# Optimization experiments

Measured on AMD Instinct MI355X. Metric: run time of the kernel, lower is better.

The kernel has to match this reference:

```python
import math
import jax, jax.numpy as jnp
import numpy as np

B, L, D = 8, 512, 1024
H, HD = 16, 64  # num_heads, head_dim (proj_dim = D)
ALPHA = 0.02       # target_alpha, warmup_steps=0 -> alpha_eff = 0.02 (< max_alpha)
STEPS = 4          # diffusion_steps
EPS = 1e-6         # _eps for float32
EARLY = 1e-5       # early_stop_eps
TEMP = 1.0

def setup_inputs() -> dict:
    key = jax.random.key(0)
    ks = jax.random.split(key, 5)
    def w(k):
        return jax.random.normal(k, (D, D), jnp.float32) * 0.02
    return {
        "hidden_states": jax.random.normal(ks[0], (B, L, D), jnp.float32),
        "Wq": w(ks[1]), "bq": jnp.zeros((D,), jnp.float32),
        "Wk": w(ks[2]), "bk": jnp.zeros((D,), jnp.float32),
        "Wv": w(ks[3]), "bv": jnp.zeros((D,), jnp.float32),
        "Wo": w(ks[4]), "bo": jnp.zeros((D,), jnp.float32),
    }

def _forward(hidden_states, Wq, bq, Wk, bk, Wv, bv, Wo, bo):
    Bn, Lq, _ = hidden_states.shape
    # projections -> (B, H, L, HD)
    Q = (hidden_states @ Wq + bq).reshape(Bn, Lq, H, HD).transpose(0, 2, 1, 3)
    K = (hidden_states @ Wk + bk).reshape(Bn, Lq, H, HD).transpose(0, 2, 1, 3)
    V = (hidden_states @ Wv + bv).reshape(Bn, Lq, H, HD).transpose(0, 2, 1, 3)
    # baseline attention p0 (no mask)
    scores = jnp.einsum('bhqd,bhkd->bhqk', Q, K) / math.sqrt(HD)
    p0 = jax.nn.softmax(scores, axis=-1)
    # key-based transition matrix P (cosine similarity, full mode)
    Kn = K / jnp.maximum(jnp.linalg.norm(K, axis=-1, keepdims=True), EPS)
    sim = jnp.einsum('bhid,bhjd->bhij', Kn, Kn) / max(1.0, math.sqrt(HD)) / TEMP
    P = jax.nn.softmax(sim, axis=-1)
    P = P * (1.0 - EPS) + EPS / P.shape[-1]  # jitter
    # iterative diffusion: p <- (1-a)*p0 + a * p @ P, with early stopping
    p = p0
    prev = p0
    done = jnp.array(False)
    for i in range(STEPS):
        p_next = (1.0 - ALPHA) * p0 + ALPHA * jnp.einsum('bhqk,bhkj->bhqj', p, P)
        if i == 0:
            cond = jnp.array(False)
        else:
            cond = jnp.max(jnp.abs(p_next - prev)) < EARLY
        new_p = jnp.where(done, p, p_next)
        new_prev = jnp.where(done | cond, prev, p)
        done = done | cond
        p, prev = new_p, new_prev
    # attention output
    attn = jnp.einsum('bhqk,bhkd->bhqd', p, V)
    attn = attn.transpose(0, 2, 1, 3).reshape(Bn, Lq, H * HD)
    return attn @ Wo + bo

def reference(hidden_states, Wq, bq, Wk, bk, Wv, bv, Wo, bo):
    return _forward(hidden_states, Wq, bq, Wk, bk, Wv, bv, Wo, bo)
```

## Files before the change

### kernel.cpp

```cpp
#include <hip/hip_runtime.h>
#include <stdint.h>

#define B_ 8
#define L_ 512
#define D_ 1024
#define H_ 16
#define HD_ 64
#define BH_ (B_*H_)
#define NR_ (B_*L_)
#define ALPHA_ 0.02f
#define PSTR 72

typedef unsigned int u32;
typedef unsigned short u16;
typedef __attribute__((ext_vector_type(8))) short bf16x8;
typedef __attribute__((ext_vector_type(4))) float f32x4;

#define MFMA16(a, b, c) __builtin_amdgcn_mfma_f32_16x16x32_bf16((a), (b), (c), 0, 0, 0)

__device__ __forceinline__ u32 f2bf_rne(float f) {
    u32 x = __float_as_uint(f);
    return (x + 0x7fffu + ((x >> 16) & 1u)) >> 16;
}
__device__ __forceinline__ float bf_lo(u32 u) { return __uint_as_float(u << 16); }
__device__ __forceinline__ float bf_hi(u32 u) { return __uint_as_float(u & 0xffff0000u); }

__device__ __forceinline__ void pack4_store(float4 v, u16* p) {
    uint2 u;
    u.x = f2bf_rne(v.x) | (f2bf_rne(v.y) << 16);
    u.y = f2bf_rne(v.z) | (f2bf_rne(v.w) << 16);
    *(uint2*)p = u;
}

__device__ __forceinline__ void gl_lds16(const u16* g, u16* l) {
    auto gp = reinterpret_cast<const __attribute__((address_space(1))) void*>(
        reinterpret_cast<uintptr_t>(g));
    auto lp = reinterpret_cast<__attribute__((address_space(3))) void*>(
        reinterpret_cast<uintptr_t>(l));
    __builtin_amdgcn_global_load_lds(gp, lp, 16, 0, 0);
}

__device__ __forceinline__ void stage8_swz(const u16* g, size_t gpitch, u16* lds, int lane) {
    const int lrow = lane >> 3;
    const int su = (lane & 7) ^ lrow;
    gl_lds16(&g[(size_t)lrow * gpitch + su * 8], lds);
}

__global__ __launch_bounds__(256) void cast_bf16(
    const float* __restrict__ src, u16* __restrict__ dst, int n8)
{
    int i = blockIdx.x * 256 + threadIdx.x;
    if (i < n8) {
        float4 a = ((const float4*)src)[(size_t)i * 2];
        float4 b = ((const float4*)src)[(size_t)i * 2 + 1];
        uint4 o;
        o.x = f2bf_rne(a.x) | (f2bf_rne(a.y) << 16);
        o.y = f2bf_rne(a.z) | (f2bf_rne(a.w) << 16);
        o.z = f2bf_rne(b.x) | (f2bf_rne(b.y) << 16);
        o.w = f2bf_rne(b.z) | (f2bf_rne(b.w) << 16);
        ((uint4*)dst)[i] = o;
    }
}

__global__ __launch_bounds__(256) void wT_bf16(
    const float* __restrict__ W0, const float* __restrict__ W1,
    const float* __restrict__ W2, const float* __restrict__ W3,
    u16* __restrict__ WTh)
{
    __shared__ float Ws[64][65];
    const int wsel = blockIdx.z;
    const float* W = (wsel == 0) ? W0 : (wsel == 1) ? W1 : (wsel == 2) ? W2 : W3;
    const int k0 = blockIdx.x * 64, n0 = blockIdx.y * 64;
    const int t = threadIdx.x;
    {
        const int r = t >> 2, c0 = (t & 3) << 4;
        #pragma unroll
        for (int i = 0; i < 4; ++i)
            *(float4*)&Ws[r][c0 + i * 4] = *(const float4*)&W[(size_t)(k0 + r) * 1024 + n0 + c0 + i * 4];
    }
    __syncthreads();
    {
        const int n = t >> 2, kc0 = (t & 3) << 4;
        size_t base = ((size_t)wsel << 20) + (size_t)(n0 + n) * 1024 + k0 + kc0;
        #pragma unroll
        for (int j = 0; j < 4; ++j) {
            float4 v;
            v.x = Ws[kc0 + j * 4 + 0][n]; v.y = Ws[kc0 + j * 4 + 1][n];
            v.z = Ws[kc0 + j * 4 + 2][n]; v.w = Ws[kc0 + j * 4 + 3][n];
            pack4_store(v, &WTh[base + j * 4]);
        }
    }
}

template<int TERMS>
__global__ __launch_bounds__(256) void gemm_mfma(
    const u16* __restrict__ Ah, const u16* __restrict__ Al,
    const u16* __restrict__ WTh,
    const float* __restrict__ b0, const float* __restrict__ b1, const float* __restrict__ b2,
    float* __restrict__ Cf, u16* __restrict__ Ch,
    u16* __restrict__ Kn, u16* __restrict__ VdT, int qkv_mode)
{
    __shared__ u16 Ash[128 * 64];
    __shared__ u16 Als[TERMS == 2 ? 128 * 64 : 8];
    __shared__ u16 Bsh[128 * 64];
    const int bm = blockIdx.x;
    const int which = blockIdx.y >> 3;
    const int bn = blockIdx.y & 7;
    const float* bias = (which == 0) ? b0 : (which == 1) ? b1 : b2;
    const int t = threadIdx.x;
    const int w = t >> 6, lane = t & 63, l15 = lane & 15, g = lane >> 4;
    const int wr = w >> 1, wc = w & 1;
    const int row0 = bm * 128, col0 = bn * 128;
    const u16* Bg = WTh + ((size_t)which << 20);
    const int r7 = l15 & 7;

    f32x4 acc[4][4];
    #pragma unroll
    for (int i = 0; i < 4; ++i)
        #pragma unroll
        for (int j = 0; j < 4; ++j) acc[i][j] = (f32x4){0.f, 0.f, 0.f, 0.f};

    for (int kt = 0; kt < 1024; kt += 64) {
        __syncthreads();
        #pragma unroll
        for (int q = 0; q < 4; ++q) {
            const int rb = w * 32 + q * 8;
            stage8_swz(&Ah[(size_t)(row0 + rb) * 1024 + kt], 1024, &Ash[rb * 64], lane);
            if constexpr (TERMS == 2)
                stage8_swz(&Al[(size_t)(row0 + rb) * 1024 + kt], 1024, &Als[rb * 64], lane);
            stage8_swz(&Bg[(size_t)(col0 + rb) * 1024 + kt], 1024, &Bsh[rb * 64], lane);
        }
        __syncthreads();
        #pragma unroll
        for (int c = 0; c < 2; ++c) {
            const int uo = ((c * 4 + g) ^ r7) * 8;
            bf16x8 ah[4], al[4], bh[4];
            #pragma unroll
            for (int mf = 0; mf < 4; ++mf) {
                const int ro = (wr * 64 + mf * 16 + l15) * 64 + uo;
                ah[mf] = *(const bf16x8*)&Ash[ro];
                if constexpr (TERMS == 2) al[mf] = *(const bf16x8*)&Als[ro];
            }
            #pragma unroll
            for (int nf = 0; nf < 4; ++nf)
                bh[nf] = *(const bf16x8*)&Bsh[(wc * 64 + nf * 16 + l15) * 64 + uo];
            #pragma unroll
            for (int mf = 0; mf < 4; ++mf)
                #pragma unroll
                for (int nf = 0; nf < 4; ++nf) {
                    acc[mf][nf] = MFMA16(ah[mf], bh[nf], acc[mf][nf]);
                    if constexpr (TERMS == 2)
                        acc[mf][nf] = MFMA16(al[mf], bh[nf], acc[mf][nf]);
                }
        }
    }

    if (!qkv_mode) {
        #pragma unroll
        for (int mf = 0; mf < 4; ++mf)
            #pragma unroll
            for (int nf = 0; nf < 4; ++nf) {
                const int n = col0 + wc * 64 + nf * 16 + l15;
                const float bv = bias[n];
                #pragma unroll
                for (int r = 0; r < 4; ++r) {
                    const int m = row0 + wr * 64 + mf * 16 + g * 4 + r;
                    Cf[(size_t)m * 1024 + n] = acc[mf][nf][r] + bv;
                }
            }
        return;
    }
    if (which == 0) {
        #pragma unroll
        for (int mf = 0; mf < 4; ++mf)
            #pragma unroll
            for (int nf = 0; nf < 4; ++nf) {
                const int n = col0 + wc * 64 + nf * 16 + l15;
                const float bv = bias[n];
                #pragma unroll
                for (int r = 0; r < 4; ++r) {
                    const int m = row0 + wr * 64 + mf * 16 + g * 4 + r;
                    Ch[(size_t)m * 1024 + n] = (u16)f2bf_rne(acc[mf][nf][r] + bv);
                }
            }
    } else if (which == 1) {
        #pragma unroll
        for (int mf = 0; mf < 4; ++mf) {
            float v[4][4];
            float sq[4] = {0.f, 0.f, 0.f, 0.f};
            #pragma unroll
            for (int nf = 0; nf < 4; ++nf) {
                const int n = col0 + wc * 64 + nf * 16 + l15;
                const float bv = bias[n];
                #pragma unroll
                for (int r = 0; r < 4; ++r) {
                    v[nf][r] = acc[mf][nf][r] + bv;
                    sq[r] += v[nf][r] * v[nf][r];
                }
            }
            #pragma unroll
            for (int r = 0; r < 4; ++r) {
                sq[r] += __shfl_xor(sq[r], 1);
                sq[r] += __shfl_xor(sq[r], 2);
                sq[r] += __shfl_xor(sq[r], 4);
                sq[r] += __shfl_xor(sq[r], 8);
            }
            float rn[4];
            #pragma unroll
            for (int r = 0; r < 4; ++r)
                rn[r] = 1.f / fmaxf(sqrtf(sq[r]), 1e-6f);
            #pragma unroll
            for (int nf = 0; nf < 4; ++nf) {
                const int n = col0 + wc * 64 + nf * 16 + l15;
                #pragma unroll
                for (int r = 0; r < 4; ++r) {
                    const int m = row0 + wr * 64 + mf * 16 + g * 4 + r;
                    Ch[((size_t)1 << 22) + (size_t)m * 1024 + n] = (u16)f2bf_rne(v[nf][r]);
                    Kn[(size_t)m * 1024 + n] = (u16)f2bf_rne(v[nf][r] * rn[r]);
                }
            }
        }
    } else {
        #pragma unroll
        for (int mf = 0; mf < 4; ++mf) {
            const int m0 = row0 + wr * 64 + mf * 16 + g * 4;
            const int bb = m0 >> 9, l0v = m0 & 511;
            #pragma unroll
            for (int nf = 0; nf < 4; ++nf) {
                const int n = col0 + wc * 64 + nf * 16 + l15;
                const float bv = bias[n];
                const int hh = n >> 6, dd = n & 63;
                const size_t idx = (((size_t)(bb * 16 + hh) * 64 + dd) * 512) + l0v;
                uint2 u;
                u.x = f2bf_rne(acc[mf][nf][0] + bv) | (f2bf_rne(acc[mf][nf][1] + bv) << 16);
                u.y = f2bf_rne(acc[mf][nf][2] + bv) | (f2bf_rne(acc[mf][nf][3] + bv) << 16);
                *(uint2*)&VdT[idx] = u;
            }
        }
    }
}

__global__ __launch_bounds__(256) void qgfd_mfma(
    const u16* __restrict__ Kn_g, const u16* __restrict__ VdT,
    u16* __restrict__ WhT)
{
    __shared__ u16 Rs[64 * 64];
    __shared__ u16 Js[64 * 64];
    __shared__ u16 Vs[64 * 64];
    __shared__ u16 Eh[4][16 * PSTR];
    const int bh = blockIdx.y, b = bh >> 4, h = bh & 15;
    const int r0 = blockIdx.x * 64;
    const int t = threadIdx.x;
    const int w = t >> 6, lane = t & 63, l15 = lane & 15, g = lane >> 4;
    const int r7 = l15 & 7;

    #pragma unroll
    for (int q = 0; q < 2; ++q) {
        const int rb = w * 16 + q * 8;
        stage8_swz(&Kn_g[((size_t)(b * 512 + r0 + rb)) * 1024 + h * 64], 1024,
                   &Rs[rb * 64], lane);
    }
    __syncthreads();
    bf16x8 rbf[2];
    rbf[0] = *(const bf16x8*)&Rs[(w * 16 + l15) * 64 + ((g ^ r7) * 8)];
    rbf[1] = *(const bf16x8*)&Rs[(w * 16 + l15) * 64 + (((4 + g) ^ r7) * 8)];

    float rsum = 0.f;
    f32x4 O[4] = {{0,0,0,0},{0,0,0,0},{0,0,0,0},{0,0,0,0}};

    for (int jt = 0; jt < 512; jt += 64) {
        __syncthreads();
        #pragma unroll
        for (int q = 0; q < 2; ++q) {
            const int rb = w * 16 + q * 8;
            stage8_swz(&Kn_g[((size_t)(b * 512 + jt + rb)) * 1024 + h * 64], 1024,
                       &Js[rb * 64], lane);
            stage8_swz(&VdT[((size_t)(bh * 64 + rb)) * 512 + jt], 512,
                       &Vs[rb * 64], lane);
        }
        __syncthreads();
        #pragma unroll
        for (int tk = 0; tk < 4; ++tk) {
            f32x4 a = {0.f, 0.f, 0.f, 0.f};
            #pragma unroll
            for (int c = 0; c < 2; ++c) {
                bf16x8 ka = *(const bf16x8*)&Js[(tk * 16 + l15) * 64 + (((c * 4 + g) ^ r7) * 8)];
                a = MFMA16(ka, rbf[c], a);
            }
            const float e0 = __expf(a[0] * 0.125f);
            const float e1 = __expf(a[1] * 0.125f);
            const float e2 = __expf(a[2] * 0.125f);
            const float e3 = __expf(a[3] * 0.125f);
            rsum += e0 + e1 + e2 + e3;
            uint2 u;
            u.x = f2bf_rne(e0) | (f2bf_rne(e1) << 16);
            u.y = f2bf_rne(e2) | (f2bf_rne(e3) << 16);
            *(uint2*)&Eh[w][l15 * PSTR + tk * 16 + g * 4] = u;
        }
        bf16x8 pah[2];
        pah[0] = *(const bf16x8*)&Eh[w][l15 * PSTR + 8 * g];
        pah[1] = *(const bf16x8*)&Eh[w][l15 * PSTR + 32 + 8 * g];
        #pragma unroll
        for (int td = 0; td < 4; ++td) {
            #pragma unroll
            for (int c = 0; c < 2; ++c) {
                bf16x8 vb = *(const bf16x8*)&Vs[(td * 16 + l15) * 64 + (((c * 4 + g) ^ r7) * 8)];
                O[td] = MFMA16(pah[c], vb, O[td]);
            }
        }
    }
    rsum += __shfl_xor(rsum, 16);
    rsum += __shfl_xor(rsum, 32);
    const float dinv = (1.0f - 1e-6f) / rsum;
    float dv[4];
    #pragma unroll
    for (int r = 0; r < 4; ++r) dv[r] = __shfl(dinv, g * 4 + r) * ALPHA_;
    #pragma unroll
    for (int td = 0; td < 4; ++td) {
        const int d = td * 16 + l15;
        const size_t idx = ((size_t)bh * 64 + d) * 512 + r0 + w * 16 + g * 4;
        uint2 vv = *(const uint2*)&VdT[idx];
        uint2 wu;
        wu.x = f2bf_rne((1.0f - ALPHA_) * bf_lo(vv.x) + dv[0] * O[td][0])
             | (f2bf_rne((1.0f - ALPHA_) * bf_hi(vv.x) + dv[1] * O[td][1]) << 16);
        wu.y = f2bf_rne((1.0f - ALPHA_) * bf_lo(vv.y) + dv[2] * O[td][2])
             | (f2bf_rne((1.0f - ALPHA_) * bf_hi(vv.y) + dv[3] * O[td][3]) << 16);
        *(uint2*)&WhT[idx] = wu;
    }
}

__global__ __launch_bounds__(256) void attn_mfma(
    const u16* __restrict__ Qh_g, const u16* __restrict__ Kh_g,
    const u16* __restrict__ Wh_g,
    u16* __restrict__ attnh, u16* __restrict__ attnl)
{
    __shared__ u16 Qs[64 * 64];
    __shared__ u16 Ks[64 * 64];
    __shared__ u16 Wsh[64 * 64];
    __shared__ u16 Ph[4][16 * PSTR];
    const int bh = blockIdx.y, b = bh >> 4, h = bh & 15;
    const int q0 = blockIdx.x * 64;
    const int t = threadIdx.x;
    const int w = t >> 6, lane = t & 63, l15 = lane & 15, g = lane >> 4;
    const int r7 = l15 & 7;

    #pragma unroll
    for (int q = 0; q < 2; ++q) {
        const int rb = w * 16 + q * 8;
        stage8_swz(&Qh_g[((size_t)(b * 512 + q0 + rb)) * 1024 + h * 64], 1024,
                   &Qs[rb * 64], lane);
    }
    __syncthreads();
    bf16x8 qbh[2];
    qbh[0] = *(const bf16x8*)&Qs[(w * 16 + l15) * 64 + ((g ^ r7) * 8)];
    qbh[1] = *(const bf16x8*)&Qs[(w * 16 + l15) * 64 + (((4 + g) ^ r7) * 8)];

    float m_run = -1e30f, l_run = 0.f;
    f32x4 O[4] = {{0,0,0,0},{0,0,0,0},{0,0,0,0},{0,0,0,0}};

    for (int kt = 0; kt < 512; kt += 64) {
        __syncthreads();
        #pragma unroll
        for (int q = 0; q < 2; ++q) {
            const int rb = w * 16 + q * 8;
            stage8_swz(&Kh_g[((size_t)(b * 512 + kt + rb)) * 1024 + h * 64], 1024,
                       &Ks[rb * 64], lane);
            stage8_swz(&Wh_g[((size_t)(bh * 64 + rb)) * 512 + kt], 512,
                       &Wsh[rb * 64], lane);
        }
        __syncthreads();
        f32x4 st[4];
        #pragma unroll
        for (int tk = 0; tk < 4; ++tk) {
            f32x4 a = {0.f, 0.f, 0.f, 0.f};
            #pragma unroll
            for (int c = 0; c < 2; ++c) {
                bf16x8 kah = *(const bf16x8*)&Ks[(tk * 16 + l15) * 64 + (((c * 4 + g) ^ r7) * 8)];
                a = MFMA16(kah, qbh[c], a);
            }
            st[tk] = a;
        }
        float mt = st[0][0];
        #pragma unroll
        for (int tk = 0; tk < 4; ++tk)
            #pragma unroll
            for (int r = 0; r < 4; ++r) mt = fmaxf(mt, st[tk][r]);
        mt = fmaxf(mt, __shfl_xor(mt, 16));
        mt = fmaxf(mt, __shfl_xor(mt, 32));
        const float m_new = fmaxf(m_run, mt);
        const float scale = __expf((m_run - m_new) * 0.125f);
        float rsum = 0.f;
        #pragma unroll
        for (int tk = 0; tk < 4; ++tk) {
            float p0_ = __expf((st[tk][0] - m_new) * 0.125f);
            float p1_ = __expf((st[tk][1] - m_new) * 0.125f);
            float p2_ = __expf((st[tk][2] - m_new) * 0.125f);
            float p3_ = __expf((st[tk][3] - m_new) * 0.125f);
            rsum += p0_ + p1_ + p2_ + p3_;
            uint2 hw;
            hw.x = f2bf_rne(p0_) | (f2bf_rne(p1_) << 16);
            hw.y = f2bf_rne(p2_) | (f2bf_rne(p3_) << 16);
            *(uint2*)&Ph[w][l15 * PSTR + tk * 16 + g * 4] = hw;
        }
        rsum += __shfl_xor(rsum, 16);
        rsum += __shfl_xor(rsum, 32);
        l_run = l_run * scale + rsum;
        m_run = m_new;
        float sc[4];
        #pragma unroll
        for (int r = 0; r < 4; ++r) sc[r] = __shfl(scale, g * 4 + r);
        #pragma unroll
        for (int td = 0; td < 4; ++td)
            #pragma unroll
            for (int r = 0; r < 4; ++r) O[td][r] *= sc[r];
        bf16x8 pah[2];
        pah[0] = *(const bf16x8*)&Ph[w][l15 * PSTR + 8 * g];
        pah[1] = *(const bf16x8*)&Ph[w][l15 * PSTR + 32 + 8 * g];
        #pragma unroll
        for (int td = 0; td < 4; ++td) {
            #pragma unroll
            for (int c = 0; c < 2; ++c) {
                bf16x8 wbh = *(const bf16x8*)&Wsh[(td * 16 + l15) * 64 + (((c * 4 + g) ^ r7) * 8)];
                O[td] = MFMA16(pah[c], wbh, O[td]);
            }
        }
    }
    const float linv = 1.f / l_run;
    float li[4];
    #pragma unroll
    for (int r = 0; r < 4; ++r) li[r] = __shfl(linv, g * 4 + r);
    #pragma unroll
    for (int td = 0; td < 4; ++td)
        #pragma unroll
        for (int r = 0; r < 4; ++r) {
            const float v = O[td][r] * li[r];
            const size_t idx = ((size_t)(b * 512 + q0 + w * 16 + g * 4 + r)) * 1024
                             + h * 64 + td * 16 + l15;
            const u32 hh = f2bf_rne(v);
            attnh[idx] = (u16)hh;
            attnl[idx] = (u16)f2bf_rne(v - bf_lo(hh));
        }
}

extern "C" void kernel_launch(void* const* d_in, const int* in_sizes, int n_in,
                              void* d_out, int out_size, void* d_ws, size_t ws_size,
                              hipStream_t stream) {
    const float* X  = (const float*)d_in[0];
    const float* Wq = (const float*)d_in[1];
    const float* bq = (const float*)d_in[2];
    const float* Wk = (const float*)d_in[3];
    const float* bk = (const float*)d_in[4];
    const float* Wv = (const float*)d_in[5];
    const float* bv = (const float*)d_in[6];
    const float* Wo = (const float*)d_in[7];
    const float* bo = (const float*)d_in[8];
    float* out = (float*)d_out;

    char* ws = (char*)d_ws;
    size_t off = 0;
    auto alloc = [&](size_t bytes) -> void* {
        void* p = ws + off;
        off += (bytes + 255) & ~(size_t)255;
        return p;
    };
    const size_t NE = (size_t)NR_ * D_;
    const size_t HE = (size_t)BH_ * 64 * 512;
    u16*   Xh    = (u16*)alloc(NE * 2);
    u16*   WTh   = (u16*)alloc((size_t)4 * 1024 * 1024 * 2);
    u16*   QKh   = (u16*)alloc(2 * NE * 2);
    u16*   Kn    = (u16*)alloc(NE * 2);
    u16*   VdT   = (u16*)alloc(HE * 2);
    u16*   WhT   = (u16*)alloc(HE * 2);
    u16*   attnh = (u16*)alloc(NE * 2);
    u16*   attnl = (u16*)alloc(NE * 2);

    const u16* Qh_g = QKh;
    const u16* Kh_g = QKh + NE;

    dim3 blk(256);
    cast_bf16<<<dim3(2048), blk, 0, stream>>>(X, Xh, (int)(NE / 8));
    wT_bf16<<<dim3(16, 16, 4), blk, 0, stream>>>(Wq, Wk, Wv, Wo, WTh);
    gemm_mfma<1><<<dim3(32, 24), blk, 0, stream>>>(Xh, nullptr, WTh, bq, bk, bv,
                                                   nullptr, QKh, Kn, VdT, 1);
    qgfd_mfma<<<dim3(8, BH_), blk, 0, stream>>>(Kn, VdT, WhT);
    attn_mfma<<<dim3(8, BH_), blk, 0, stream>>>(Qh_g, Kh_g, WhT, attnh, attnl);
    gemm_mfma<2><<<dim3(32, 8), blk, 0, stream>>>(attnh, attnl,
                                                  WTh + ((size_t)3 << 20),
                                                  bo, bo, bo, out, nullptr,
                                                  nullptr, nullptr, 0);
}
```

Measured before the change: 140.1 us.

## Process 128 rows per block in diffusion and attention kernels; fuse prep casts

```diff
diff --git a/kernel.cpp b/kernel.cpp
--- a/kernel.cpp
+++ b/kernel.cpp
@@ -46,32 +46,33 @@
     gl_lds16(&g[(size_t)lrow * gpitch + su * 8], lds);
 }
 
-__global__ __launch_bounds__(256) void cast_bf16(
-    const float* __restrict__ src, u16* __restrict__ dst, int n8)
-{
-    int i = blockIdx.x * 256 + threadIdx.x;
-    if (i < n8) {
-        float4 a = ((const float4*)src)[(size_t)i * 2];
-        float4 b = ((const float4*)src)[(size_t)i * 2 + 1];
-        uint4 o;
-        o.x = f2bf_rne(a.x) | (f2bf_rne(a.y) << 16);
-        o.y = f2bf_rne(a.z) | (f2bf_rne(a.w) << 16);
-        o.z = f2bf_rne(b.x) | (f2bf_rne(b.y) << 16);
-        o.w = f2bf_rne(b.z) | (f2bf_rne(b.w) << 16);
-        ((uint4*)dst)[i] = o;
-    }
-}
-
-__global__ __launch_bounds__(256) void wT_bf16(
+__global__ __launch_bounds__(256) void prep_kernel(
+    const float* __restrict__ X, u16* __restrict__ Xh,
     const float* __restrict__ W0, const float* __restrict__ W1,
     const float* __restrict__ W2, const float* __restrict__ W3,
     u16* __restrict__ WTh)
 {
+    const int t = threadIdx.x;
+    if (blockIdx.z == 4) {
+        const int cid = blockIdx.y * 16 + blockIdx.x;
+        #pragma unroll
+        for (int i = 0; i < 8; ++i) {
+            const int n8 = cid * 2048 + i * 256 + t;
+            float4 a = ((const float4*)X)[(size_t)n8 * 2];
+            float4 b = ((const float4*)X)[(size_t)n8 * 2 + 1];
+            uint4 o;
+            o.x = f2bf_rne(a.x) | (f2bf_rne(a.y) << 16);
+            o.y = f2bf_rne(a.z) | (f2bf_rne(a.w) << 16);
+            o.z = f2bf_rne(b.x) | (f2bf_rne(b.y) << 16);
+            o.w = f2bf_rne(b.z) | (f2bf_rne(b.w) << 16);
+            ((uint4*)Xh)[n8] = o;
+        }
+        return;
+    }
     __shared__ float Ws[64][65];
     const int wsel = blockIdx.z;
     const float* W = (wsel == 0) ? W0 : (wsel == 1) ? W1 : (wsel == 2) ? W2 : W3;
     const int k0 = blockIdx.x * 64, n0 = blockIdx.y * 64;
-    const int t = threadIdx.x;
     {
         const int r = t >> 2, c0 = (t & 3) << 4;
         #pragma unroll
@@ -244,29 +245,33 @@
     const u16* __restrict__ Kn_g, const u16* __restrict__ VdT,
     u16* __restrict__ WhT)
 {
-    __shared__ u16 Rs[64 * 64];
+    __shared__ u16 Rs[128 * 64];
     __shared__ u16 Js[64 * 64];
     __shared__ u16 Vs[64 * 64];
     __shared__ u16 Eh[4][16 * PSTR];
     const int bh = blockIdx.y, b = bh >> 4, h = bh & 15;
-    const int r0 = blockIdx.x * 64;
+    const int r0 = blockIdx.x * 128;
     const int t = threadIdx.x;
     const int w = t >> 6, lane = t & 63, l15 = lane & 15, g = lane >> 4;
     const int r7 = l15 & 7;
 
     #pragma unroll
-    for (int q = 0; q < 2; ++q) {
-        const int rb = w * 16 + q * 8;
+    for (int q = 0; q < 4; ++q) {
+        const int rb = w * 32 + q * 8;
         stage8_swz(&Kn_g[((size_t)(b * 512 + r0 + rb)) * 1024 + h * 64], 1024,
                    &Rs[rb * 64], lane);
     }
     __syncthreads();
-    bf16x8 rbf[2];
-    rbf[0] = *(const bf16x8*)&Rs[(w * 16 + l15) * 64 + ((g ^ r7) * 8)];
-    rbf[1] = *(const bf16x8*)&Rs[(w * 16 + l15) * 64 + (((4 + g) ^ r7) * 8)];
-
-    float rsum = 0.f;
-    f32x4 O[4] = {{0,0,0,0},{0,0,0,0},{0,0,0,0},{0,0,0,0}};
+    bf16x8 rbf[2][2];
+    #pragma unroll
+    for (int rt = 0; rt < 2; ++rt) {
+        rbf[rt][0] = *(const bf16x8*)&Rs[(rt * 64 + w * 16 + l15) * 64 + ((g ^ r7) * 8)];
+        rbf[rt][1] = *(const bf16x8*)&Rs[(rt * 64 + w * 16 + l15) * 64 + (((4 + g) ^ r7) * 8)];
+    }
+
+    float rsum[2] = {0.f, 0.f};
+    f32x4 O[2][4] = {{{0,0,0,0},{0,0,0,0},{0,0,0,0},{0,0,0,0}},
+                     {{0,0,0,0},{0,0,0,0},{0,0,0,0},{0,0,0,0}}};
 
     for (int jt = 0; jt < 512; jt += 64) {
         __syncthreads();
@@ -280,52 +285,59 @@
         }
         __syncthreads();
         #pragma unroll
-        for (int tk = 0; tk < 4; ++tk) {
-            f32x4 a = {0.f, 0.f, 0.f, 0.f};
-            #pragma unroll
-            for (int c = 0; c < 2; ++c) {
-                bf16x8 ka = *(const bf16x8*)&Js[(tk * 16 + l15) * 64 + (((c * 4 + g) ^ r7) * 8)];
-                a = MFMA16(ka, rbf[c], a);
-            }
-            const float e0 = __expf(a[0] * 0.125f);
-            const float e1 = __expf(a[1] * 0.125f);
-            const float e2 = __expf(a[2] * 0.125f);
-            const float e3 = __expf(a[3] * 0.125f);
-            rsum += e0 + e1 + e2 + e3;
-            uint2 u;
-            u.x = f2bf_rne(e0) | (f2bf_rne(e1) << 16);
-            u.y = f2bf_rne(e2) | (f2bf_rne(e3) << 16);
-            *(uint2*)&Eh[w][l15 * PSTR + tk * 16 + g * 4] = u;
-        }
-        bf16x8 pah[2];
-        pah[0] = *(const bf16x8*)&Eh[w][l15 * PSTR + 8 * g];
-        pah[1] = *(const bf16x8*)&Eh[w][l15 * PSTR + 32 + 8 * g];
+        for (int rt = 0; rt < 2; ++rt) {
+            #pragma unroll
+            for (int tk = 0; tk < 4; ++tk) {
+                f32x4 a = {0.f, 0.f, 0.f, 0.f};
+                #pragma unroll
+                for (int c = 0; c < 2; ++c) {
+                    bf16x8 ka = *(const bf16x8*)&Js[(tk * 16 + l15) * 64 + (((c * 4 + g) ^ r7) * 8)];
+                    a = MFMA16(ka, rbf[rt][c], a);
+                }
+                const float e0 = __expf(a[0] * 0.125f);
+                const float e1 = __expf(a[1] * 0.125f);
+                const float e2 = __expf(a[2] * 0.125f);
+                const float e3 = __expf(a[3] * 0.125f);
+                rsum[rt] += e0 + e1 + e2 + e3;
+                uint2 u;
+                u.x = f2bf_rne(e0) | (f2bf_rne(e1) << 16);
+                u.y = f2bf_rne(e2) | (f2bf_rne(e3) << 16);
+                *(uint2*)&Eh[w][l15 * PSTR + tk * 16 + g * 4] = u;
+            }
+            bf16x8 pah[2];
+            pah[0] = *(const bf16x8*)&Eh[w][l15 * PSTR + 8 * g];
+            pah[1] = *(const bf16x8*)&Eh[w][l15 * PSTR + 32 + 8 * g];
+            #pragma unroll
+            for (int td = 0; td < 4; ++td) {
+                #pragma unroll
+                for (int c = 0; c < 2; ++c) {
+                    bf16x8 vb = *(const bf16x8*)&Vs[(td * 16 + l15) * 64 + (((c * 4 + g) ^ r7) * 8)];
+                    O[rt][td] = MFMA16(pah[c], vb, O[rt][td]);
+                }
+            }
+        }
+    }
+    #pragma unroll
+    for (int rt = 0; rt < 2; ++rt) {
+        float rs = rsum[rt];
+        rs += __shfl_xor(rs, 16);
+        rs += __shfl_xor(rs, 32);
+        const float dinv = (1.0f - 1e-6f) / rs;
+        float dv[4];
+        #pragma unroll
+        for (int r = 0; r < 4; ++r) dv[r] = __shfl(dinv, g * 4 + r) * ALPHA_;
         #pragma unroll
         for (int td = 0; td < 4; ++td) {
-            #pragma unroll
-            for (int c = 0; c < 2; ++c) {
-                bf16x8 vb = *(const bf16x8*)&Vs[(td * 16 + l15) * 64 + (((c * 4 + g) ^ r7) * 8)];
-                O[td] = MFMA16(pah[c], vb, O[td]);
-            }
-        }
-    }
-    rsum += __shfl_xor(rsum, 16);
-    rsum += __shfl_xor(rsum, 32);
-    const float dinv = (1.0f - 1e-6f) / rsum;
-    float dv[4];
-    #pragma unroll
-    for (int r = 0; r < 4; ++r) dv[r] = __shfl(dinv, g * 4 + r) * ALPHA_;
-    #pragma unroll
-    for (int td = 0; td < 4; ++td) {
-        const int d = td * 16 + l15;
-        const size_t idx = ((size_t)bh * 64 + d) * 512 + r0 + w * 16 + g * 4;
-        uint2 vv = *(const uint2*)&VdT[idx];
-        uint2 wu;
-        wu.x = f2bf_rne((1.0f - ALPHA_) * bf_lo(vv.x) + dv[0] * O[td][0])
-             | (f2bf_rne((1.0f - ALPHA_) * bf_hi(vv.x) + dv[1] * O[td][1]) << 16);
-        wu.y = f2bf_rne((1.0f - ALPHA_) * bf_lo(vv.y) + dv[2] * O[td][2])
-             | (f2bf_rne((1.0f - ALPHA_) * bf_hi(vv.y) + dv[3] * O[td][3]) << 16);
-        *(uint2*)&WhT[idx] = wu;
+            const int d = td * 16 + l15;
+            const size_t idx = ((size_t)bh * 64 + d) * 512 + r0 + rt * 64 + w * 16 + g * 4;
+            uint2 vv = *(const uint2*)&VdT[idx];
+            uint2 wu;
+            wu.x = f2bf_rne((1.0f - ALPHA_) * bf_lo(vv.x) + dv[0] * O[rt][td][0])
+                 | (f2bf_rne((1.0f - ALPHA_) * bf_hi(vv.x) + dv[1] * O[rt][td][1]) << 16);
+            wu.y = f2bf_rne((1.0f - ALPHA_) * bf_lo(vv.y) + dv[2] * O[rt][td][2])
+                 | (f2bf_rne((1.0f - ALPHA_) * bf_hi(vv.y) + dv[3] * O[rt][td][3]) << 16);
+            *(uint2*)&WhT[idx] = wu;
+        }
     }
 }
 
@@ -334,29 +346,33 @@
     const u16* __restrict__ Wh_g,
     u16* __restrict__ attnh, u16* __restrict__ attnl)
 {
-    __shared__ u16 Qs[64 * 64];
+    __shared__ u16 Qs[128 * 64];
     __shared__ u16 Ks[64 * 64];
     __shared__ u16 Wsh[64 * 64];
     __shared__ u16 Ph[4][16 * PSTR];
     const int bh = blockIdx.y, b = bh >> 4, h = bh & 15;
-    const int q0 = blockIdx.x * 64;
+    const int q0 = blockIdx.x * 128;
     const int t = threadIdx.x;
     const int w = t >> 6, lane = t & 63, l15 = lane & 15, g = lane >> 4;
     const int r7 = l15 & 7;
 
     #pragma unroll
-    for (int q = 0; q < 2; ++q) {
-        const int rb = w * 16 + q * 8;
+    for (int q = 0; q < 4; ++q) {
+        const int rb = w * 32 + q * 8;
         stage8_swz(&Qh_g[((size_t)(b * 512 + q0 + rb)) * 1024 + h * 64], 1024,
                    &Qs[rb * 64], lane);
     }
     __syncthreads();
-    bf16x8 qbh[2];
-    qbh[0] = *(const bf16x8*)&Qs[(w * 16 + l15) * 64 + ((g ^ r7) * 8)];
-    qbh[1] = *(const bf16x8*)&Qs[(w * 16 + l15) * 64 + (((4 + g) ^ r7) * 8)];
-
-    float m_run = -1e30f, l_run = 0.f;
-    f32x4 O[4] = {{0,0,0,0},{0,0,0,0},{0,0,0,0},{0,0,0,0}};
+    bf16x8 qbh[2][2];
+    #pragma unroll
+    for (int qt = 0; qt < 2; ++qt) {
+        qbh[qt][0] = *(const bf16x8*)&Qs[(qt * 64 + w * 16 + l15) * 64 + ((g ^ r7) * 8)];
+        qbh[qt][1] = *(const bf16x8*)&Qs[(qt * 64 + w * 16 + l15) * 64 + (((4 + g) ^ r7) * 8)];
+    }
+
+    float m_run[2] = {-1e30f, -1e30f}, l_run[2] = {0.f, 0.f};
+    f32x4 O[2][4] = {{{0,0,0,0},{0,0,0,0},{0,0,0,0},{0,0,0,0}},
+                     {{0,0,0,0},{0,0,0,0},{0,0,0,0},{0,0,0,0}}};
 
     for (int kt = 0; kt < 512; kt += 64) {
         __syncthreads();
@@ -369,77 +385,83 @@
                        &Wsh[rb * 64], lane);
         }
         __syncthreads();
-        f32x4 st[4];
-        #pragma unroll
-        for (int tk = 0; tk < 4; ++tk) {
-            f32x4 a = {0.f, 0.f, 0.f, 0.f};
-            #pragma unroll
-            for (int c = 0; c < 2; ++c) {
-                bf16x8 kah = *(const bf16x8*)&Ks[(tk * 16 + l15) * 64 + (((c * 4 + g) ^ r7) * 8)];
-                a = MFMA16(kah, qbh[c], a);
-            }
-            st[tk] = a;
-        }
-        float mt = st[0][0];
-        #pragma unroll
-        for (int tk = 0; tk < 4; ++tk)
-            #pragma unroll
-            for (int r = 0; r < 4; ++r) mt = fmaxf(mt, st[tk][r]);
-        mt = fmaxf(mt, __shfl_xor(mt, 16));
-        mt = fmaxf(mt, __shfl_xor(mt, 32));
-        const float m_new = fmaxf(m_run, mt);
-        const float scale = __expf((m_run - m_new) * 0.125f);
-        float rsum = 0.f;
-        #pragma unroll
-        for (int tk = 0; tk < 4; ++tk) {
-            float p0_ = __expf((st[tk][0] - m_new) * 0.125f);
-            float p1_ = __expf((st[tk][1] - m_new) * 0.125f);
-            float p2_ = __expf((st[tk][2] - m_new) * 0.125f);
-            float p3_ = __expf((st[tk][3] - m_new) * 0.125f);
-            rsum += p0_ + p1_ + p2_ + p3_;
-            uint2 hw;
-            hw.x = f2bf_rne(p0_) | (f2bf_rne(p1_) << 16);
-            hw.y = f2bf_rne(p2_) | (f2bf_rne(p3_) << 16);
-            *(uint2*)&Ph[w][l15 * PSTR + tk * 16 + g * 4] = hw;
-        }
-        rsum += __shfl_xor(rsum, 16);
-        rsum += __shfl_xor(rsum, 32);
-        l_run = l_run * scale + rsum;
-        m_run = m_new;
-        float sc[4];
-        #pragma unroll
-        for (int r = 0; r < 4; ++r) sc[r] = __shfl(scale, g * 4 + r);
+        #pragma unroll
+        for (int qt = 0; qt < 2; ++qt) {
+            f32x4 st[4];
+            #pragma unroll
+            for (int tk = 0; tk < 4; ++tk) {
+                f32x4 a = {0.f, 0.f, 0.f, 0.f};
+                #pragma unroll
+                for (int c = 0; c < 2; ++c) {
+                    bf16x8 kah = *(const bf16x8*)&Ks[(tk * 16 + l15) * 64 + (((c * 4 + g) ^ r7) * 8)];
+                    a = MFMA16(kah, qbh[qt][c], a);
+                }
+                st[tk] = a;
+            }
+            float mt = st[0][0];
+            #pragma unroll
+            for (int tk = 0; tk < 4; ++tk)
+                #pragma unroll
+                for (int r = 0; r < 4; ++r) mt = fmaxf(mt, st[tk][r]);
+            mt = fmaxf(mt, __shfl_xor(mt, 16));
+            mt = fmaxf(mt, __shfl_xor(mt, 32));
+            const float m_new = fmaxf(m_run[qt], mt);
+            const float scale = __expf((m_run[qt] - m_new) * 0.125f);
+            float rsum = 0.f;
+            #pragma unroll
+            for (int tk = 0; tk < 4; ++tk) {
+                float p0_ = __expf((st[tk][0] - m_new) * 0.125f);
+                float p1_ = __expf((st[tk][1] - m_new) * 0.125f);
+                float p2_ = __expf((st[tk][2] - m_new) * 0.125f);
+                float p3_ = __expf((st[tk][3] - m_new) * 0.125f);
+                rsum += p0_ + p1_ + p2_ + p3_;
+                uint2 hw;
+                hw.x = f2bf_rne(p0_) | (f2bf_rne(p1_) << 16);
+                hw.y = f2bf_rne(p2_) | (f2bf_rne(p3_) << 16);
+                *(uint2*)&Ph[w][l15 * PSTR + tk * 16 + g * 4] = hw;
+            }
+            rsum += __shfl_xor(rsum, 16);
+            rsum += __shfl_xor(rsum, 32);
+            l_run[qt] = l_run[qt] * scale + rsum;
+            m_run[qt] = m_new;
+            float sc[4];
+            #pragma unroll
+            for (int r = 0; r < 4; ++r) sc[r] = __shfl(scale, g * 4 + r);
+            #pragma unroll
+            for (int td = 0; td < 4; ++td)
+                #pragma unroll
+                for (int r = 0; r < 4; ++r) O[qt][td][r] *= sc[r];
+            bf16x8 pah[2];
+            pah[0] = *(const bf16x8*)&Ph[w][l15 * PSTR + 8 * g];
+            pah[1] = *(const bf16x8*)&Ph[w][l15 * PSTR + 32 + 8 * g];
+            #pragma unroll
+            for (int td = 0; td < 4; ++td) {
+                #pragma unroll
+                for (int c = 0; c < 2; ++c) {
+                    bf16x8 wbh = *(const bf16x8*)&Wsh[(td * 16 + l15) * 64 + (((c * 4 + g) ^ r7) * 8)];
+                    O[qt][td] = MFMA16(pah[c], wbh, O[qt][td]);
+                }
+            }
+        }
+    }
+    #pragma unroll
+    for (int qt = 0; qt < 2; ++qt) {
+        const float linv = 1.f / l_run[qt];
+        float li[4];
+        #pragma unroll
+        for (int r = 0; r < 4; ++r) li[r] = __shfl(linv, g * 4 + r);
         #pragma unroll
         for (int td = 0; td < 4; ++td)
             #pragma unroll
-            for (int r = 0; r < 4; ++r) O[td][r] *= sc[r];
-        bf16x8 pah[2];
-        pah[0] = *(const bf16x8*)&Ph[w][l15 * PSTR + 8 * g];
-        pah[1] = *(const bf16x8*)&Ph[w][l15 * PSTR + 32 + 8 * g];
-        #pragma unroll
-        for (int td = 0; td < 4; ++td) {
-            #pragma unroll
-            for (int c = 0; c < 2; ++c) {
-                bf16x8 wbh = *(const bf16x8*)&Wsh[(td * 16 + l15) * 64 + (((c * 4 + g) ^ r7) * 8)];
-                O[td] = MFMA16(pah[c], wbh, O[td]);
-            }
-        }
-    }
-    const float linv = 1.f / l_run;
-    float li[4];
-    #pragma unroll
-    for (int r = 0; r < 4; ++r) li[r] = __shfl(linv, g * 4 + r);
-    #pragma unroll
-    for (int td = 0; td < 4; ++td)
-        #pragma unroll
-        for (int r = 0; r < 4; ++r) {
-            const float v = O[td][r] * li[r];
-            const size_t idx = ((size_t)(b * 512 + q0 + w * 16 + g * 4 + r)) * 1024
-                             + h * 64 + td * 16 + l15;
-            const u32 hh = f2bf_rne(v);
-            attnh[idx] = (u16)hh;
-            attnl[idx] = (u16)f2bf_rne(v - bf_lo(hh));
-        }
+            for (int r = 0; r < 4; ++r) {
+                const float v = O[qt][td][r] * li[r];
+                const size_t idx = ((size_t)(b * 512 + q0 + qt * 64 + w * 16 + g * 4 + r)) * 1024
+                                 + h * 64 + td * 16 + l15;
+                const u32 hh = f2bf_rne(v);
+                attnh[idx] = (u16)hh;
+                attnl[idx] = (u16)f2bf_rne(v - bf_lo(hh));
+            }
+    }
 }
 
 extern "C" void kernel_launch(void* const* d_in, const int* in_sizes, int n_in,
@@ -478,12 +500,11 @@
     const u16* Kh_g = QKh + NE;
 
     dim3 blk(256);
-    cast_bf16<<<dim3(2048), blk, 0, stream>>>(X, Xh, (int)(NE / 8));
-    wT_bf16<<<dim3(16, 16, 4), blk, 0, stream>>>(Wq, Wk, Wv, Wo, WTh);
+    prep_kernel<<<dim3(16, 16, 5), blk, 0, stream>>>(X, Xh, Wq, Wk, Wv, Wo, WTh);
     gemm_mfma<1><<<dim3(32, 24), blk, 0, stream>>>(Xh, nullptr, WTh, bq, bk, bv,
                                                    nullptr, QKh, Kn, VdT, 1);
-    qgfd_mfma<<<dim3(8, BH_), blk, 0, stream>>>(Kn, VdT, WhT);
-    attn_mfma<<<dim3(8, BH_), blk, 0, stream>>>(Qh_g, Kh_g, WhT, attnh, attnl);
+    qgfd_mfma<<<dim3(4, BH_), blk, 0, stream>>>(Kn, VdT, WhT);
+    attn_mfma<<<dim3(4, BH_), blk, 0, stream>>>(Qh_g, Kh_g, WhT, attnh, attnl);
     gemm_mfma<2><<<dim3(32, 8), blk, 0, stream>>>(attnh, attnl,
                                                   WTh + ((size_t)3 << 20),
                                                   bo, bo, bo, out, nullptr,
```

Result: faster. 133.4 us (-4.8%).
